# Kernel tuning notes

Measured on AMD Instinct MI355X. Metric: run time of the kernel, lower is better.

## Reference

```python
import jax, jax.numpy as jnp
import numpy as np
import math

H = 16          # num_attention_heads
D = 64          # attention_head_size
MAX_POS = 1024  # max_position_embeddings


def setup_inputs() -> dict:
    key = jax.random.key(0)
    ks = jax.random.split(key, 6)
    B, S, HID = 4, 1024, 1024
    scale = 1.0 / math.sqrt(HID)
    return {
        "hidden_states": jax.random.normal(ks[0], (B, S, HID), jnp.float32),
        "attention_mask": jnp.zeros((B, 1, 1, S), jnp.float32),
        "Wq": jax.random.normal(ks[1], (HID, HID), jnp.float32) * scale,
        "bq": jnp.zeros((HID,), jnp.float32),
        "Wk": jax.random.normal(ks[2], (HID, HID), jnp.float32) * scale,
        "bk": jnp.zeros((HID,), jnp.float32),
        "Wv": jax.random.normal(ks[3], (HID, HID), jnp.float32) * scale,
        "bv": jnp.zeros((HID,), jnp.float32),
        "dist_emb": jax.random.normal(ks[4], (2 * MAX_POS - 1, D), jnp.float32) * 0.02,
    }


def _split_heads(x):
    # [B,S,H*D] -> [B,H,S,D]
    B, S, _ = x.shape
    return x.reshape(B, S, H, D).transpose(0, 2, 1, 3)


def reference(hidden_states, attention_mask, Wq, bq, Wk, bk, Wv, bv, dist_emb):
    B, S, _ = hidden_states.shape
    q = _split_heads(hidden_states @ Wq.T + bq)   # [B,H,S,D]
    k = _split_heads(hidden_states @ Wk.T + bk)
    v = _split_heads(hidden_states @ Wv.T + bv)

    scores = jnp.einsum("bhqd,bhkd->bhqk", q, k)  # [B,H,S,S]

    # relative_key_query positional bias
    pos_l = jnp.arange(S)[:, None]
    pos_r = jnp.arange(S)[None, :]
    distance = pos_l - pos_r + (MAX_POS - 1)      # [S,S] in [0, 2*MAX_POS-2]
    pos_emb = dist_emb[distance]                  # [S,S,D]
    rel_q = jnp.einsum("bhld,lrd->bhlr", q, pos_emb)
    rel_k = jnp.einsum("bhrd,lrd->bhlr", k, pos_emb)
    scores = (scores + rel_q + rel_k) / math.sqrt(D)

    scores = scores + attention_mask
    probs = jax.nn.softmax(scores, axis=-1)
    ctx = jnp.einsum("bhqk,bhkd->bhqd", probs, v)  # [B,H,S,D]
    ctx = ctx.transpose(0, 2, 1, 3).reshape(B, S, H * D)
    return ctx
```

## Files before the change

### kernel.cpp

```cpp
#include <hip/hip_runtime.h>
#include <hip/hip_bf16.h>

#define B_   4
#define S_   1024
#define HID_ 1024
#define H_   16
#define D_   64

typedef __attribute__((ext_vector_type(4))) float f32x4;
typedef __attribute__((ext_vector_type(8))) __bf16 bf16v8;
typedef __attribute__((ext_vector_type(8))) unsigned short u16x8;
typedef __attribute__((ext_vector_type(4))) unsigned short u16x4;

#define MFMA16(a, b, c) __builtin_amdgcn_mfma_f32_16x16x32_bf16((a), (b), (c), 0, 0, 0)
#define GLOAD16(gp, lp)                                                              \
    __builtin_amdgcn_global_load_lds((const __attribute__((address_space(1))) void*)(gp), \
                                     (__attribute__((address_space(3))) void*)(lp), 16, 0, 0)

__device__ __forceinline__ unsigned short f2bs_hw(float f) {
    __bf16 h = (__bf16)f;
    return __builtin_bit_cast(unsigned short, h);
}
__device__ __forceinline__ unsigned pack2bf(float a, float b) {
    unsigned short lo = f2bs_hw(a), hi = f2bs_hw(b);
    return (unsigned)lo | ((unsigned)hi << 16);
}
__device__ __forceinline__ float bs2f(unsigned short s) {
    union { unsigned u; float f; } v; v.u = ((unsigned)s) << 16;
    return v.f;
}

__global__ void convall_kernel(const float* __restrict__ X,
                               const float* __restrict__ Wq, const float* __restrict__ Wk,
                               const float* __restrict__ Wv, const float* __restrict__ E,
                               unsigned short* __restrict__ Xb,
                               unsigned short* __restrict__ Wqb, unsigned short* __restrict__ Wkb,
                               unsigned short* __restrict__ Wvb, unsigned short* __restrict__ Eb) {
    int bid = blockIdx.x;
    const float* src;
    unsigned short* dst;
    int n4, base;
    if (bid < 4096)      { src = X;  dst = Xb;  n4 = 1048576; base = bid; }
    else if (bid < 5120) { src = Wq; dst = Wqb; n4 = 262144;  base = bid - 4096; }
    else if (bid < 6144) { src = Wk; dst = Wkb; n4 = 262144;  base = bid - 5120; }
    else if (bid < 7168) { src = Wv; dst = Wvb; n4 = 262144;  base = bid - 6144; }
    else                 { src = E;  dst = Eb;  n4 = 32752;   base = bid - 7168; }
    int i = base * 256 + threadIdx.x;
    if (i < n4) {
        float4 x = *(const float4*)(src + (size_t)i * 4);
        uint2 o;
        o.x = pack2bf(x.x, x.y);
        o.y = pack2bf(x.z, x.w);
        *(uint2*)(dst + (size_t)i * 4) = o;
    }
}

__global__ __launch_bounds__(256)
void proj_kernel(const unsigned short* __restrict__ Xb,
                 const unsigned short* __restrict__ Wqb, const float* __restrict__ bq,
                 const unsigned short* __restrict__ Wkb, const float* __restrict__ bk,
                 const unsigned short* __restrict__ Wvb, const float* __restrict__ bv,
                 unsigned short* __restrict__ Qo, unsigned short* __restrict__ Ko,
                 unsigned short* __restrict__ Vo)
{
    __shared__ __align__(16) unsigned short Al[2][128][64];
    __shared__ __align__(16) unsigned short Bl[2][128][64];

    const int bid = blockIdx.x;
    const int tile = (bid & 7) * 96 + (bid >> 3);
    const int rt = tile / 24, ct = tile % 24;
    const int row0 = rt * 128, col0 = ct * 128;
    const int which = col0 >> 10;
    const unsigned short* Wm = (which == 0) ? Wqb : (which == 1) ? Wkb : Wvb;
    const float* bias        = (which == 0) ? bq  : (which == 1) ? bk  : bv;
    unsigned short* Out      = (which == 0) ? Qo  : (which == 1) ? Ko  : Vo;
    const int oc0 = col0 & 1023;

    const int t = threadIdx.x;
    const int lane = t & 63, w = t >> 6;
    const int wr = w >> 1, wc = w & 1;
    const int lg = lane >> 4, lc = lane & 15;

    f32x4 acc[4][4] = {};

#pragma unroll
    for (int l = 0; l < 4; ++l) {
        int idx = l * 256 + t;
        int r = idx >> 3, su = idx & 7;
        int u = su ^ (r & 7);
        GLOAD16(Xb + (size_t)(row0 + r) * 1024 + u * 8,
                &Al[0][0][0] + (size_t)(l * 256 + w * 64) * 8);
        GLOAD16(Wm + (size_t)(oc0 + r) * 1024 + u * 8,
                &Bl[0][0][0] + (size_t)(l * 256 + w * 64) * 8);
    }

    for (int it = 0; it < 16; ++it) {
        const int p = it & 1;
        __syncthreads();
        if (it < 15) {
            const int k1 = (it + 1) * 64;
#pragma unroll
            for (int l = 0; l < 4; ++l) {
                int idx = l * 256 + t;
                int r = idx >> 3, su = idx & 7;
                int u = su ^ (r & 7);
                GLOAD16(Xb + (size_t)(row0 + r) * 1024 + k1 + u * 8,
                        &Al[p ^ 1][0][0] + (size_t)(l * 256 + w * 64) * 8);
                GLOAD16(Wm + (size_t)(oc0 + r) * 1024 + k1 + u * 8,
                        &Bl[p ^ 1][0][0] + (size_t)(l * 256 + w * 64) * 8);
            }
        }
        bf16v8 af[4][2], bfg[4][2];
#pragma unroll
        for (int m = 0; m < 4; ++m)
#pragma unroll
            for (int ks = 0; ks < 2; ++ks) {
                int u = (ks * 4 + lg) ^ (lc & 7);
                af[m][ks] = *(const bf16v8*)&Al[p][wr * 64 + m * 16 + lc][u * 8];
            }
#pragma unroll
        for (int n = 0; n < 4; ++n)
#pragma unroll
            for (int ks = 0; ks < 2; ++ks) {
                int u = (ks * 4 + lg) ^ (lc & 7);
                bfg[n][ks] = *(const bf16v8*)&Bl[p][wc * 64 + n * 16 + lc][u * 8];
            }
        __builtin_amdgcn_s_setprio(1);
#pragma unroll
        for (int m = 0; m < 4; ++m)
#pragma unroll
            for (int n = 0; n < 4; ++n) {
                acc[m][n] = MFMA16(af[m][0], bfg[n][0], acc[m][n]);
                acc[m][n] = MFMA16(af[m][1], bfg[n][1], acc[m][n]);
            }
        __builtin_amdgcn_s_setprio(0);
    }

#pragma unroll
    for (int m = 0; m < 4; ++m)
#pragma unroll
        for (int n = 0; n < 4; ++n) {
            int j = oc0 + wc * 64 + n * 16 + lc;
            int hh = j >> 6, dd = j & 63;
            float bv_ = bias[j];
#pragma unroll
            for (int r = 0; r < 4; ++r) {
                int i = row0 + wr * 64 + m * 16 + lg * 4 + r;
                int bb = i >> 10, ss = i & 1023;
                float v = acc[m][n][r] + bv_;
                Out[((size_t)(bb * 16 + hh) * 1024 + ss) * 64 + dd] = f2bs_hw(v);
            }
        }
}

__global__ __launch_bounds__(256)
void attn_kernel(const unsigned short* __restrict__ Q,
                 const unsigned short* __restrict__ K,
                 const unsigned short* __restrict__ V,
                 const float* __restrict__ mask,
                 const unsigned short* __restrict__ Eb,
                 float* __restrict__ Out)
{
    __shared__ __align__(16) unsigned short Kl[64][64];
    __shared__ __align__(16) unsigned short El[128][64];
    __shared__ __align__(16) unsigned short VTl[64][72];
    __shared__ __align__(16) unsigned short QDl[4][16][136];
    __shared__ __align__(16) unsigned short KDl[64][132];
    __shared__ __align__(16) unsigned Pex[4 * 16 * 36];
    __shared__ float maskl[64];

    const int t = threadIdx.x;
    const int lane = t & 63, w = t >> 6;
    const int lg = lane >> 4, lc = lane & 15;

    const int bid = blockIdx.x;
    const int bh = bid & 63;
    const int qt = bid >> 6;
    const int b = bh >> 4, h = bh & 15;
    const int i0 = qt * 64;
    const int i_loc = w * 16 + lc;

    const float C2 = 0.125f * 1.44269504089f;
    const float L2E = 1.44269504089f;

    const unsigned short* Qh = Q + (size_t)bh * S_ * D_;
    const unsigned short* Kh = K + (size_t)bh * S_ * D_;
    const unsigned short* Vh = V + (size_t)bh * S_ * D_;

    bf16v8 qf[2];
#pragma unroll
    for (int ks = 0; ks < 2; ++ks)
        qf[ks] = *(const bf16v8*)(Qh + (size_t)(i0 + i_loc) * D_ + ks * 32 + lg * 8);

    u16x8 ones_u;
#pragma unroll
    for (int e = 0; e < 8; ++e) ones_u[e] = 0x3F80;
    const bf16v8 onesf = __builtin_bit_cast(bf16v8, ones_u);

    float m_r = -1e30f;
    f32x4 lacc = (f32x4){0.f, 0.f, 0.f, 0.f};
    f32x4 ctx[4];
#pragma unroll
    for (int nd = 0; nd < 4; ++nd) ctx[nd] = (f32x4){0.f, 0.f, 0.f, 0.f};

    unsigned* PexW = &Pex[(w * 16 + lc) * 36];

    const int va = t & 7, vrb = (t >> 3) << 1;
    const int vcq = va * 8;
    const int vjst = (vrb + (va << 3)) & 63;

    u16x8 v0c, v1c;
    float mkc;
    {
#pragma unroll
        for (int l = 0; l < 2; ++l) {
            int idx = l * 256 + t;
            int r = idx >> 3, su = idx & 7;
            int u = su ^ (r & 7);
            GLOAD16(Kh + (size_t)r * 64 + u * 8,
                    &Kl[0][0] + (size_t)(l * 256 + w * 64) * 8);
        }
        const int db0 = i0 + 960;
        const int sb0 = db0 & 127;
#pragma unroll
        for (int l = 0; l < 4; ++l) {
            int idx = l * 256 + t;
            int sl = idx >> 3, su = idx & 7;
            int u = su ^ (sl & 7);
            int dr = db0 + ((sl - sb0) & 127);
            if (dr > 2046) dr = 2046;
            GLOAD16(Eb + (size_t)dr * 64 + u * 8,
                    &El[0][0] + (size_t)(l * 256 + w * 64) * 8);
        }
        v0c = *(const u16x8*)(Vh + (size_t)vrb * 64 + vcq);
        v1c = *(const u16x8*)(Vh + (size_t)(vrb + 1) * 64 + vcq);
        mkc = (t < 64) ? mask[(size_t)b * S_ + t] * L2E : 0.f;
    }

    for (int jt = 0; jt < 16; ++jt) {
        const int j0 = jt * 64;
        const int dbase = i0 - j0 + 960;
        __syncthreads();

#pragma unroll
        for (int e = 0; e < 8; ++e)
            *(unsigned*)&VTl[vcq + e][vjst] = (unsigned)v0c[e] | ((unsigned)v1c[e] << 16);
        if (t < 64) maskl[t] = mkc;
        __syncthreads();

        bf16v8 kfa[2];
#pragma unroll
        for (int ks = 0; ks < 2; ++ks) {
            int u = (ks * 4 + lg) ^ (lc & 7);
            kfa[ks] = *(const bf16v8*)&Kl[w * 16 + lc][u * 8];
        }
        __builtin_amdgcn_s_setprio(1);
#pragma unroll
        for (int nd = 0; nd < 8; ++nd) {
            int sl = (dbase + nd * 16 + lc) & 127;
            int u0 = lg ^ (lc & 7);
            int u1 = (4 + lg) ^ (lc & 7);
            bf16v8 ef0 = *(const bf16v8*)&El[sl][u0 * 8];
            bf16v8 ef1 = *(const bf16v8*)&El[sl][u1 * 8];
            f32x4 kd = (f32x4){0.f, 0.f, 0.f, 0.f};
            kd = MFMA16(ef0, kfa[0], kd);
            kd = MFMA16(ef1, kfa[1], kd);
            uint2 pk;
            pk.x = pack2bf(kd[0], kd[1]);
            pk.y = pack2bf(kd[2], kd[3]);
            *(uint2*)&KDl[w * 16 + lc][nd * 16 + lg * 4] = pk;
            if (nd < 4 || jt == 0) {
                f32x4 qd = (f32x4){0.f, 0.f, 0.f, 0.f};
                qd = MFMA16(ef0, qf[0], qd);
                qd = MFMA16(ef1, qf[1], qd);
                int slot0 = ((dbase & 127) + nd * 16 + lg * 4) & 127;
                uint2 qk2;
                qk2.x = pack2bf(qd[0], qd[1]);
                qk2.y = pack2bf(qd[2], qd[3]);
                *(uint2*)&QDl[w][lc][slot0] = qk2;
            }
        }
        f32x4 s[4];
#pragma unroll
        for (int n = 0; n < 4; ++n) {
            s[n] = (f32x4){0.f, 0.f, 0.f, 0.f};
#pragma unroll
            for (int ks = 0; ks < 2; ++ks) {
                int u = (ks * 4 + lg) ^ (lc & 7);
                bf16v8 kb = *(const bf16v8*)&Kl[n * 16 + lc][u * 8];
                s[n] = MFMA16(kb, qf[ks], s[n]);
            }
        }
        __builtin_amdgcn_s_setprio(0);
        __syncthreads();

        if (jt < 15) {
            const int j0n = j0 + 64;
            const int dbn = dbase - 64;
            const int sbn = dbn & 127;
#pragma unroll
            for (int l = 0; l < 2; ++l) {
                int idx = l * 256 + t;
                int r = idx >> 3, su = idx & 7;
                int u = su ^ (r & 7);
                GLOAD16(Kh + (size_t)(j0n + r) * 64 + u * 8,
                        &Kl[0][0] + (size_t)(l * 256 + w * 64) * 8);
            }
#pragma unroll
            for (int l = 0; l < 2; ++l) {
                int idx = l * 256 + t;
                int rl = idx >> 3, su = idx & 7;
                int u = su ^ (rl & 7);
                GLOAD16(Eb + (size_t)(dbn + rl) * 64 + u * 8,
                        &El[sbn][0] + (size_t)(l * 256 + w * 64) * 8);
            }
            v0c = *(const u16x8*)(Vh + (size_t)(j0n + vrb) * 64 + vcq);
            v1c = *(const u16x8*)(Vh + (size_t)(j0n + vrb + 1) * 64 + vcq);
            mkc = (t < 64) ? mask[(size_t)b * S_ + j0n + t] * L2E : 0.f;
        }

        const unsigned short* QDw = &QDl[w][lc][0];
        float vmax = -1e30f;
#pragma unroll
        for (int n = 0; n < 4; ++n) {
            int jb = n * 16 + lg * 4;
            float4 mk = *(const float4*)&maskl[jb];
            int kbase = jb * 131 + i_loc + 63;
            int qbase = dbase + i_loc - jb + 63;
#pragma unroll
            for (int r = 0; r < 4; ++r) {
                float qdv = bs2f(QDw[(qbase - r) & 127]);
                float kdv = bs2f((&KDl[0][0])[kbase + 131 * r]);
                float mkr = (r == 0) ? mk.x : (r == 1) ? mk.y : (r == 2) ? mk.z : mk.w;
                float val = (s[n][r] + qdv + kdv) * C2 + mkr;
                s[n][r] = val;
                vmax = fmaxf(vmax, val);
            }
        }
        vmax = fmaxf(vmax, __shfl_xor(vmax, 16));
        vmax = fmaxf(vmax, __shfl_xor(vmax, 32));

        if (__any(vmax > m_r)) {
            float mnew = fmaxf(m_r, vmax);
            float alpha = exp2f(m_r - mnew);
            m_r = mnew;
#pragma unroll
            for (int r = 0; r < 4; ++r) lacc[r] *= alpha;
#pragma unroll
            for (int nd = 0; nd < 4; ++nd)
#pragma unroll
                for (int r = 0; r < 4; ++r)
                    ctx[nd][r] *= alpha;
        }

#pragma unroll
        for (int n = 0; n < 4; ++n)
#pragma unroll
            for (int r = 0; r < 4; ++r)
                s[n][r] = exp2f(s[n][r] - m_r);

#pragma unroll
        for (int n = 0; n < 4; ++n) {
            uint2 pk;
            pk.x = pack2bf(s[n][0], s[n][1]);
            pk.y = pack2bf(s[n][2], s[n][3]);
            *(uint2*)&PexW[n * 8 + lg * 2] = pk;
        }
        bf16v8 pfB[2];
#pragma unroll
        for (int ks = 0; ks < 2; ++ks) {
            int nc = 2 * ks + (lg >> 1);
            pfB[ks] = *(const bf16v8*)&PexW[nc * 8 + (lg & 1) * 4];
        }

        __builtin_amdgcn_s_setprio(1);
        lacc = MFMA16(onesf, pfB[0], lacc);
        lacc = MFMA16(onesf, pfB[1], lacc);
#pragma unroll
        for (int nd = 0; nd < 4; ++nd) {
            int vrow = nd * 16 + lc;
#pragma unroll
            for (int ks = 0; ks < 2; ++ks) {
                int jst = (ks * 32 + lg * 8 + ((vrow >> 3) << 3)) & 63;
                bf16v8 vf = *(const bf16v8*)&VTl[vrow][jst];
                ctx[nd] = MFMA16(vf, pfB[ks], ctx[nd]);
            }
        }
        __builtin_amdgcn_s_setprio(0);
    }

    float inv = 1.0f / lacc[0];
    float* outp = Out + ((size_t)(b * S_ + i0 + i_loc) * H_ + h) * D_;
#pragma unroll
    for (int nd = 0; nd < 4; ++nd) {
        float4 o;
        o.x = ctx[nd][0] * inv;
        o.y = ctx[nd][1] * inv;
        o.z = ctx[nd][2] * inv;
        o.w = ctx[nd][3] * inv;
        *(float4*)(outp + nd * 16 + lg * 4) = o;
    }
}

extern "C" void kernel_launch(void* const* d_in, const int* in_sizes, int n_in,
                              void* d_out, int out_size, void* d_ws, size_t ws_size,
                              hipStream_t stream)
{
    const float* X    = (const float*)d_in[0];
    const float* mask = (const float*)d_in[1];
    const float* Wq   = (const float*)d_in[2];
    const float* bq   = (const float*)d_in[3];
    const float* Wk   = (const float*)d_in[4];
    const float* bk   = (const float*)d_in[5];
    const float* Wv   = (const float*)d_in[6];
    const float* bv   = (const float*)d_in[7];
    const float* E    = (const float*)d_in[8];
    float* Out = (float*)d_out;

    const size_t headN = (size_t)B_ * H_ * S_ * D_;
    unsigned short* Qw  = (unsigned short*)d_ws;
    unsigned short* Kw  = Qw + headN;
    unsigned short* Vw  = Kw + headN;
    unsigned short* Ebw = Vw + headN;
    unsigned short* Xb  = Ebw + (size_t)2047 * 64;
    unsigned short* Wqb = Xb + (size_t)4096 * 1024;
    unsigned short* Wkb = Wqb + (size_t)1024 * 1024;
    unsigned short* Wvb = Wkb + (size_t)1024 * 1024;

    convall_kernel<<<dim3(7296), dim3(256), 0, stream>>>(X, Wq, Wk, Wv, E,
                                                         Xb, Wqb, Wkb, Wvb, Ebw);
    proj_kernel<<<dim3(768), dim3(256), 0, stream>>>(Xb, Wqb, bq, Wkb, bk, Wvb, bv, Qw, Kw, Vw);
    attn_kernel<<<dim3(1024), dim3(256), 0, stream>>>(Qw, Kw, Vw, mask, Ebw, Out);
}
```

Before: 149.3 us.

## Stage projection epilogue through LDS for coalesced stores; drop redundant attention barrier

The projection kernel's two LDS tiles are merged into one buffer, which is reused after the main loop to stage the biased bf16 output tile. The tile is then written to the head-split Q/K/V layout as 16-byte coalesced stores instead of scattered 2-byte stores. In the attention kernel, one barrier after the V-transpose/mask writes is removed, the QK score MFMAs are moved ahead of the positional MFMAs, and the QDl row padding shrinks from 136 to 132. Removing that barrier depends on the shared data written there not being read before the next barrier, which adds a risk of a race.

```diff
diff --git a/kernel.cpp b/kernel.cpp
--- a/kernel.cpp
+++ b/kernel.cpp
@@ -63,8 +63,7 @@
                  unsigned short* __restrict__ Qo, unsigned short* __restrict__ Ko,
                  unsigned short* __restrict__ Vo)
 {
-    __shared__ __align__(16) unsigned short Al[2][128][64];
-    __shared__ __align__(16) unsigned short Bl[2][128][64];
+    __shared__ __align__(16) unsigned short SM[4 * 128 * 64];
 
     const int bid = blockIdx.x;
     const int tile = (bid & 7) * 96 + (bid >> 3);
@@ -89,9 +88,9 @@
         int r = idx >> 3, su = idx & 7;
         int u = su ^ (r & 7);
         GLOAD16(Xb + (size_t)(row0 + r) * 1024 + u * 8,
-                &Al[0][0][0] + (size_t)(l * 256 + w * 64) * 8);
+                SM + (size_t)(l * 256 + w * 64) * 8);
         GLOAD16(Wm + (size_t)(oc0 + r) * 1024 + u * 8,
-                &Bl[0][0][0] + (size_t)(l * 256 + w * 64) * 8);
+                SM + 16384 + (size_t)(l * 256 + w * 64) * 8);
     }
 
     for (int it = 0; it < 16; ++it) {
@@ -105,9 +104,9 @@
                 int r = idx >> 3, su = idx & 7;
                 int u = su ^ (r & 7);
                 GLOAD16(Xb + (size_t)(row0 + r) * 1024 + k1 + u * 8,
-                        &Al[p ^ 1][0][0] + (size_t)(l * 256 + w * 64) * 8);
+                        SM + (p ^ 1) * 8192 + (size_t)(l * 256 + w * 64) * 8);
                 GLOAD16(Wm + (size_t)(oc0 + r) * 1024 + k1 + u * 8,
-                        &Bl[p ^ 1][0][0] + (size_t)(l * 256 + w * 64) * 8);
+                        SM + 16384 + (p ^ 1) * 8192 + (size_t)(l * 256 + w * 64) * 8);
             }
         }
         bf16v8 af[4][2], bfg[4][2];
@@ -116,14 +115,14 @@
 #pragma unroll
             for (int ks = 0; ks < 2; ++ks) {
                 int u = (ks * 4 + lg) ^ (lc & 7);
-                af[m][ks] = *(const bf16v8*)&Al[p][wr * 64 + m * 16 + lc][u * 8];
+                af[m][ks] = *(const bf16v8*)(SM + p * 8192 + (wr * 64 + m * 16 + lc) * 64 + u * 8);
             }
 #pragma unroll
         for (int n = 0; n < 4; ++n)
 #pragma unroll
             for (int ks = 0; ks < 2; ++ks) {
                 int u = (ks * 4 + lg) ^ (lc & 7);
-                bfg[n][ks] = *(const bf16v8*)&Bl[p][wc * 64 + n * 16 + lc][u * 8];
+                bfg[n][ks] = *(const bf16v8*)(SM + 16384 + p * 8192 + (wc * 64 + n * 16 + lc) * 64 + u * 8);
             }
         __builtin_amdgcn_s_setprio(1);
 #pragma unroll
@@ -136,21 +135,31 @@
         __builtin_amdgcn_s_setprio(0);
     }
 
+    __syncthreads();
+    float bvv[4];
+#pragma unroll
+    for (int n = 0; n < 4; ++n) bvv[n] = bias[oc0 + wc * 64 + n * 16 + lc];
 #pragma unroll
     for (int m = 0; m < 4; ++m)
 #pragma unroll
-        for (int n = 0; n < 4; ++n) {
-            int j = oc0 + wc * 64 + n * 16 + lc;
-            int hh = j >> 6, dd = j & 63;
-            float bv_ = bias[j];
+        for (int n = 0; n < 4; ++n)
 #pragma unroll
             for (int r = 0; r < 4; ++r) {
-                int i = row0 + wr * 64 + m * 16 + lg * 4 + r;
-                int bb = i >> 10, ss = i & 1023;
-                float v = acc[m][n][r] + bv_;
-                Out[((size_t)(bb * 16 + hh) * 1024 + ss) * 64 + dd] = f2bs_hw(v);
-            }
-        }
+                int i  = wr * 64 + m * 16 + lg * 4 + r;
+                int jj = wc * 64 + n * 16 + lc;
+                SM[i * 132 + jj] = f2bs_hw(acc[m][n][r] + bvv[n]);
+            }
+    __syncthreads();
+    const int bb = row0 >> 10, ss0 = row0 & 1023, hh0 = oc0 >> 6;
+#pragma unroll
+    for (int it = 0; it < 8; ++it) {
+        int f = it * 2048 + t * 8;
+        int ch = f >> 13, rem = f & 8191;
+        int i = rem >> 6, dd = rem & 63;
+        u16x8 v = *(const u16x8*)(SM + i * 132 + ch * 64 + dd);
+        unsigned short* op = Out + (((size_t)(bb * 16 + hh0 + ch) * 1024 + ss0 + i) * 64 + dd);
+        *(u16x8*)op = v;
+    }
 }
 
 __global__ __launch_bounds__(256)
@@ -164,7 +173,7 @@
     __shared__ __align__(16) unsigned short Kl[64][64];
     __shared__ __align__(16) unsigned short El[128][64];
     __shared__ __align__(16) unsigned short VTl[64][72];
-    __shared__ __align__(16) unsigned short QDl[4][16][136];
+    __shared__ __align__(16) unsigned short QDl[4][16][132];
     __shared__ __align__(16) unsigned short KDl[64][132];
     __shared__ __align__(16) unsigned Pex[4 * 16 * 36];
     __shared__ float maskl[64];
@@ -246,7 +255,6 @@
         for (int e = 0; e < 8; ++e)
             *(unsigned*)&VTl[vcq + e][vjst] = (unsigned)v0c[e] | ((unsigned)v1c[e] << 16);
         if (t < 64) maskl[t] = mkc;
-        __syncthreads();
 
         bf16v8 kfa[2];
 #pragma unroll
@@ -254,7 +262,19 @@
             int u = (ks * 4 + lg) ^ (lc & 7);
             kfa[ks] = *(const bf16v8*)&Kl[w * 16 + lc][u * 8];
         }
+        f32x4 s[4];
         __builtin_amdgcn_s_setprio(1);
+#pragma unroll
+        for (int n = 0; n < 4; ++n) {
+            s[n] = (f32x4){0.f, 0.f, 0.f, 0.f};
+#pragma unroll
+            for (int ks = 0; ks < 2; ++ks) {
+                int u = (ks * 4 + lg) ^ (lc & 7);
+                bf16v8 kb = *(const bf16v8*)&Kl[n * 16 + lc][u * 8];
+                s[n] = MFMA16(kb, qf[ks], s[n]);
+            }
+        }
+
 #pragma unroll
         for (int nd = 0; nd < 8; ++nd) {
             int sl = (dbase + nd * 16 + lc) & 127;
@@ -280,17 +300,6 @@
                 *(uint2*)&QDl[w][lc][slot0] = qk2;
             }
         }
-        f32x4 s[4];
-#pragma unroll
-        for (int n = 0; n < 4; ++n) {
-            s[n] = (f32x4){0.f, 0.f, 0.f, 0.f};
-#pragma unroll
-            for (int ks = 0; ks < 2; ++ks) {
-                int u = (ks * 4 + lg) ^ (lc & 7);
-                bf16v8 kb = *(const bf16v8*)&Kl[n * 16 + lc][u * 8];
-                s[n] = MFMA16(kb, qf[ks], s[n]);
-            }
-        }
         __builtin_amdgcn_s_setprio(0);
         __syncthreads();
 
```

Result: slower. 162.4 us (+8.8%).
